# Optimization experiments

Hardware: AMD Instinct MI355X
Metric: run time of the kernel (lower is better)

Reference implementation:

```python
import jax, jax.numpy as jnp
import numpy as np

B, S, D_IN, D_OUT = 4, 2048, 1024, 1024

def setup_inputs() -> dict:
    key = jax.random.key(0)
    k_x, k_q, k_k, k_v = jax.random.split(key, 4)
    return {
        "x": jax.random.normal(k_x, (B, S, D_IN), dtype=jnp.float32),
        "W_query": jax.random.uniform(k_q, (D_IN, D_OUT), dtype=jnp.float32),
        "W_key": jax.random.uniform(k_k, (D_IN, D_OUT), dtype=jnp.float32),
        "W_value": jax.random.uniform(k_v, (D_IN, D_OUT), dtype=jnp.float32),
    }

def reference(x, W_query, W_key, W_value):
    seq_len = x.shape[1]
    d_out = W_key.shape[-1]
    # fused QKV projection: x @ concat([Wq, Wk, Wv], -1), then split
    qkv = x @ jnp.concatenate([W_query, W_key, W_value], axis=-1)  # [B,S,3*d_out]
    query, key, value = jnp.split(qkv, 3, axis=2)
    # raw scores [B,S,S]; causal mask applied BEFORE scaling (as in source)
    attn_weights = jnp.einsum("bqd,bkd->bqk", query, key)
    causal = jnp.triu(jnp.ones((seq_len, seq_len), dtype=bool), k=1)
    attn_weights = jnp.where(causal[None, :, :], -jnp.inf, attn_weights)
    scaled = attn_weights / jnp.asarray(d_out, x.dtype) ** 0.5
    attn_scores = jax.nn.softmax(scaled, axis=-1)  # dropout p=0 -> identity
    context_vectors = jnp.einsum("bqk,bkd->bqd", attn_scores, value)
    return (context_vectors, attn_scores)
```

## Files before the change

kernel.cpp:

```cpp
#include <hip/hip_runtime.h>
#include <cstdint>
#include <cstddef>


#define S_LEN 2048
#define D_DIM 1024
#define NBATCH 4
#define MEG (1024 * 1024)

typedef __attribute__((ext_vector_type(4))) float floatx4;
typedef __attribute__((ext_vector_type(8))) __bf16 bf16x8;
typedef __attribute__((ext_vector_type(8))) short short8v;

__device__ __forceinline__ unsigned short f2bf(float f) {
  union { float f; unsigned u; } v; v.f = f;
  unsigned r = v.u + 0x7FFF + ((v.u >> 16) & 1);
  return (unsigned short)(r >> 16);
}
__device__ __forceinline__ float bf2f(unsigned short h) {
  union { unsigned u; float f; } v; v.u = ((unsigned)h) << 16; return v.f;
}

__device__ __forceinline__ void async_copy16(const void* g, void* l) {
  __builtin_amdgcn_global_load_lds(
      (const __attribute__((address_space(1))) void*)g,
      (__attribute__((address_space(3))) void*)l, 16, 0, 0);
}

__device__ __forceinline__ void gemm_bt_core(
    const short* __restrict__ A, const short* __restrict__ B,
    int lda, int ldb, int kIters, int blockM, int blockN,
    short (*As)[32], short (*Bs)[32], floatx4 (&acc)[4][4])
{
  const int tid  = threadIdx.x;
  const int lane = tid & 63;
  const int wave = tid >> 6;
  const int wm = (wave >> 1) * 64;
  const int wn = (wave & 1) * 64;
  const int fm = lane & 15;
  const int fk = (lane >> 4) * 8;
  const int r0 = tid >> 2;
  const int c0 = (tid & 3) * 8;

  floatx4 zero = {0.f, 0.f, 0.f, 0.f};
  #pragma unroll
  for (int i = 0; i < 4; ++i)
    #pragma unroll
    for (int j = 0; j < 4; ++j)
      acc[i][j] = zero;

  const short* a0 = A + (size_t)(blockM + r0) * lda + c0;
  const short* a1 = a0 + (size_t)64 * lda;
  const short* b0 = B + (size_t)(blockN + r0) * ldb + c0;
  const short* b1 = b0 + (size_t)64 * ldb;
  short* as0 = &As[r0][c0];
  short* as1 = &As[r0 + 64][c0];
  short* bs0 = &Bs[r0][c0];
  short* bs1 = &Bs[r0 + 64][c0];

  for (int kt = 0; kt < kIters; ++kt) {
    const int kb = kt * 32;
    async_copy16(a0 + kb, as0);
    async_copy16(a1 + kb, as1);
    async_copy16(b0 + kb, bs0);
    async_copy16(b1 + kb, bs1);
    __syncthreads();
    bf16x8 af[4], bfr[4];
    #pragma unroll
    for (int i = 0; i < 4; ++i)
      af[i] = *(const bf16x8*)(&As[wm + i * 16 + fm][fk]);
    #pragma unroll
    for (int j = 0; j < 4; ++j)
      bfr[j] = *(const bf16x8*)(&Bs[wn + j * 16 + fm][fk]);
    #pragma unroll
    for (int i = 0; i < 4; ++i)
      #pragma unroll
      for (int j = 0; j < 4; ++j)
        acc[i][j] = __builtin_amdgcn_mfma_f32_16x16x32_bf16(af[i], bfr[j], acc[i][j], 0, 0, 0);
    __syncthreads();
  }
}

__device__ __forceinline__ void gemm_bt_split_core(
    const short* __restrict__ Ah, const short* __restrict__ Al,
    const short* __restrict__ Bh, const short* __restrict__ Bl,
    int lda, int ldb, int kIters, int blockM, int blockN,
    short (*AsH)[32], short (*AsL)[32], short (*BsH)[32], short (*BsL)[32],
    floatx4 (&acc)[4][4])
{
  const int tid  = threadIdx.x;
  const int lane = tid & 63;
  const int wave = tid >> 6;
  const int wm = (wave >> 1) * 64;
  const int wn = (wave & 1) * 64;
  const int fm = lane & 15;
  const int fk = (lane >> 4) * 8;
  const int r0 = tid >> 2;
  const int c0 = (tid & 3) * 8;

  floatx4 zero = {0.f, 0.f, 0.f, 0.f};
  #pragma unroll
  for (int i = 0; i < 4; ++i)
    #pragma unroll
    for (int j = 0; j < 4; ++j)
      acc[i][j] = zero;

  const size_t oa0 = (size_t)(blockM + r0) * lda + c0;
  const size_t oa1 = oa0 + (size_t)64 * lda;
  const size_t ob0 = (size_t)(blockN + r0) * ldb + c0;
  const size_t ob1 = ob0 + (size_t)64 * ldb;
  short* lah0 = &AsH[r0][c0]; short* lah1 = &AsH[r0 + 64][c0];
  short* lal0 = &AsL[r0][c0]; short* lal1 = &AsL[r0 + 64][c0];
  short* lbh0 = &BsH[r0][c0]; short* lbh1 = &BsH[r0 + 64][c0];
  short* lbl0 = &BsL[r0][c0]; short* lbl1 = &BsL[r0 + 64][c0];

  for (int kt = 0; kt < kIters; ++kt) {
    const int kb = kt * 32;
    async_copy16(Ah + oa0 + kb, lah0);
    async_copy16(Ah + oa1 + kb, lah1);
    async_copy16(Al + oa0 + kb, lal0);
    async_copy16(Al + oa1 + kb, lal1);
    async_copy16(Bh + ob0 + kb, lbh0);
    async_copy16(Bh + ob1 + kb, lbh1);
    async_copy16(Bl + ob0 + kb, lbl0);
    async_copy16(Bl + ob1 + kb, lbl1);
    __syncthreads();
    bf16x8 ah[4], al[4], bh[4], bl[4];
    #pragma unroll
    for (int i = 0; i < 4; ++i) {
      ah[i] = *(const bf16x8*)(&AsH[wm + i * 16 + fm][fk]);
      al[i] = *(const bf16x8*)(&AsL[wm + i * 16 + fm][fk]);
    }
    #pragma unroll
    for (int j = 0; j < 4; ++j) {
      bh[j] = *(const bf16x8*)(&BsH[wn + j * 16 + fm][fk]);
      bl[j] = *(const bf16x8*)(&BsL[wn + j * 16 + fm][fk]);
    }
    #pragma unroll
    for (int i = 0; i < 4; ++i)
      #pragma unroll
      for (int j = 0; j < 4; ++j) {
        acc[i][j] = __builtin_amdgcn_mfma_f32_16x16x32_bf16(ah[i], bh[j], acc[i][j], 0, 0, 0);
        acc[i][j] = __builtin_amdgcn_mfma_f32_16x16x32_bf16(ah[i], bl[j], acc[i][j], 0, 0, 0);
        acc[i][j] = __builtin_amdgcn_mfma_f32_16x16x32_bf16(al[i], bh[j], acc[i][j], 0, 0, 0);
      }
    __syncthreads();
  }
}


__global__ __launch_bounds__(256) void k_cvt(
    const float4* __restrict__ x,
    const float* __restrict__ wq, const float* __restrict__ wk,
    const float* __restrict__ wv,
    short* __restrict__ xh, short* __restrict__ xl,
    short* __restrict__ wqh, short* __restrict__ wql,
    short* __restrict__ wkh, short* __restrict__ wkl,
    short* __restrict__ wvt)
{
  const int bid = blockIdx.x;
  const int tid = threadIdx.x;
  if (bid < 5120) {
    const float4* src;
    short *dh, *dl;
    size_t idx;
    if (bid < 4096) {
      idx = (size_t)bid * 256 + tid;
      src = x; dh = xh; dl = xl;
    } else if (bid < 4608) {
      idx = (size_t)(bid - 4096) * 256 + tid;
      src = (const float4*)wq; dh = wqh; dl = wql;
    } else {
      idx = (size_t)(bid - 4608) * 256 + tid;
      src = (const float4*)wk; dh = wkh; dl = wkl;
    }
    const float4 u4 = src[idx * 2];
    const float4 w4 = src[idx * 2 + 1];
    float f[8] = {u4.x, u4.y, u4.z, u4.w, w4.x, w4.y, w4.z, w4.w};
    short8v oh, ol;
    #pragma unroll
    for (int e = 0; e < 8; ++e) {
      const unsigned short h = f2bf(f[e]);
      oh[e] = (short)h;
      ol[e] = (short)f2bf(f[e] - bf2f(h));
    }
    *(short8v*)(dh + idx * 8) = oh;
    *(short8v*)(dl + idx * 8) = ol;
  } else {
    const int rem = bid - 5120;
    const int bx = rem & 31, by = rem >> 5;
    const int tx = tid & 31, ty = tid >> 5;
    __shared__ float tile[32][33];
    const int colIn = bx * 32 + tx;
    #pragma unroll
    for (int i = 0; i < 4; ++i) {
      const int rowIn = by * 32 + ty + i * 8;
      tile[ty + i * 8][tx] = wv[(size_t)rowIn * D_DIM + colIn];
    }
    __syncthreads();
    const int colOut = by * 32 + tx;
    #pragma unroll
    for (int i = 0; i < 4; ++i) {
      const int rowOut = bx * 32 + ty + i * 8;
      wvt[(size_t)rowOut * D_DIM + colOut] = (short)f2bf(tile[tx][ty + i * 8]);
    }
  }
}


__global__ __launch_bounds__(256) void k_gemm_m(
    const short* __restrict__ wqh, const short* __restrict__ wql,
    const short* __restrict__ wkh, const short* __restrict__ wkl,
    short* __restrict__ mth, short* __restrict__ mtl)
{
  __shared__ alignas(16) short AsH[128][32];
  __shared__ alignas(16) short AsL[128][32];
  __shared__ alignas(16) short BsH[128][32];
  __shared__ alignas(16) short BsL[128][32];
  floatx4 acc[4][4];
  const int blockM = blockIdx.y * 128;
  const int blockN = blockIdx.x * 128;
  gemm_bt_split_core(wkh, wkl, wqh, wql,
                     D_DIM, D_DIM, D_DIM / 32, blockM, blockN,
                     AsH, AsL, BsH, BsL, acc);

  const int tid = threadIdx.x, lane = tid & 63, wave = tid >> 6;
  const int wm = (wave >> 1) * 64, wn = (wave & 1) * 64;
  const int rb = wm + ((lane >> 4) << 2);
  const int cb = wn + (lane & 15);
  #pragma unroll
  for (int i = 0; i < 4; ++i)
    #pragma unroll
    for (int j = 0; j < 4; ++j) {
      const int n = blockN + cb + j * 16;
      #pragma unroll
      for (int r = 0; r < 4; ++r) {
        const int m = blockM + rb + i * 16 + r;
        const float f = acc[i][j][r];
        const unsigned short h = f2bf(f);
        mth[(size_t)m * D_DIM + n] = (short)h;
        mtl[(size_t)m * D_DIM + n] = (short)f2bf(f - bf2f(h));
      }
    }
}


__global__ __launch_bounds__(256) void k_mu(const short* __restrict__ mth,
                                            const short* __restrict__ mtl,
                                            float* __restrict__ mu) {
  const int j = blockIdx.x, tid = threadIdx.x;
  const ushort4 h = *(const ushort4*)(mth + (size_t)j * D_DIM + tid * 4);
  const ushort4 l = *(const ushort4*)(mtl + (size_t)j * D_DIM + tid * 4);
  float s = bf2f(h.x) + bf2f(l.x) + bf2f(h.y) + bf2f(l.y)
          + bf2f(h.z) + bf2f(l.z) + bf2f(h.w) + bf2f(l.w);
  #pragma unroll
  for (int off = 32; off > 0; off >>= 1) s += __shfl_xor(s, off);
  __shared__ float ps[4];
  if ((tid & 63) == 0) ps[tid >> 6] = s;
  __syncthreads();
  if (tid == 0) mu[j] = (ps[0] + ps[1] + ps[2] + ps[3]) * (1.0f / 1024.0f);
}


__global__ __launch_bounds__(256) void k_rowstats(
    const short* __restrict__ xh, const short* __restrict__ xl,
    const float* __restrict__ mu, float* __restrict__ sq, float* __restrict__ u)
{
  const int r = blockIdx.x, tid = threadIdx.x;
  const ushort4 h = *(const ushort4*)(xh + (size_t)r * D_DIM + tid * 4);
  const ushort4 l = *(const ushort4*)(xl + (size_t)r * D_DIM + tid * 4);
  const float4 m4 = *(const float4*)(mu + tid * 4);
  const float x0 = bf2f(h.x) + bf2f(l.x);
  const float x1 = bf2f(h.y) + bf2f(l.y);
  const float x2 = bf2f(h.z) + bf2f(l.z);
  const float x3 = bf2f(h.w) + bf2f(l.w);
  float s = x0 + x1 + x2 + x3;
  float uu = m4.x * x0 + m4.y * x1 + m4.z * x2 + m4.w * x3;
  #pragma unroll
  for (int off = 32; off > 0; off >>= 1) {
    s  += __shfl_xor(s, off);
    uu += __shfl_xor(uu, off);
  }
  __shared__ float ps[4], pu[4];
  if ((tid & 63) == 0) { ps[tid >> 6] = s; pu[tid >> 6] = uu; }
  __syncthreads();
  if (tid == 0) {
    sq[r] = ps[0] + ps[1] + ps[2] + ps[3];
    u[r]  = pu[0] + pu[1] + pu[2] + pu[3];
  }
}


__global__ __launch_bounds__(256) void k_gemm_n(
    const short* __restrict__ xh, const short* __restrict__ xl,
    const short* __restrict__ mth, const short* __restrict__ mtl,
    const float* __restrict__ sq, const float* __restrict__ mu,
    short* __restrict__ nh, short* __restrict__ nl)
{
  __shared__ alignas(16) short AsH[128][32];
  __shared__ alignas(16) short AsL[128][32];
  __shared__ alignas(16) short BsH[128][32];
  __shared__ alignas(16) short BsL[128][32];
  floatx4 acc[4][4];
  const int blockM = blockIdx.y * 128;
  const int blockN = blockIdx.x * 128;
  gemm_bt_split_core(xh, xl, mth, mtl, D_DIM, D_DIM, D_DIM / 32,
                     blockM, blockN, AsH, AsL, BsH, BsL, acc);

  const int tid = threadIdx.x, lane = tid & 63, wave = tid >> 6;
  const int wm = (wave >> 1) * 64, wn = (wave & 1) * 64;
  const int rb = wm + ((lane >> 4) << 2);
  const int cb = wn + (lane & 15);
  #pragma unroll
  for (int i = 0; i < 4; ++i)
    #pragma unroll
    for (int j = 0; j < 4; ++j) {
      const int n = blockN + cb + j * 16;
      const float muv = mu[n];
      #pragma unroll
      for (int r = 0; r < 4; ++r) {
        const int m = blockM + rb + i * 16 + r;
        const float f = acc[i][j][r] - sq[m] * muv;
        const unsigned short h = f2bf(f);
        nh[(size_t)m * D_DIM + n] = (short)h;
        nl[(size_t)m * D_DIM + n] = (short)f2bf(f - bf2f(h));
      }
    }
}


__global__ __launch_bounds__(256) void k_gemm_sv(
    const short* __restrict__ nh, const short* __restrict__ nl,
    const short* __restrict__ xh, const short* __restrict__ xl,
    const float* __restrict__ sq, const float* __restrict__ u,
    const short* __restrict__ wvt, float* __restrict__ attn,
    short* __restrict__ vt)
{
  __shared__ alignas(16) short AsH[128][32];
  __shared__ alignas(16) short AsL[128][32];
  __shared__ alignas(16) short BsH[128][32];
  __shared__ alignas(16) short BsL[128][32];
  floatx4 acc[4][4];
  const int bid = blockIdx.x;
  const int tid = threadIdx.x, lane = tid & 63, wave = tid >> 6;
  const int wm = (wave >> 1) * 64, wn = (wave & 1) * 64;
  const int rb = wm + ((lane >> 4) << 2);
  const int cb = wn + (lane & 15);

  if (bid < 544) {
    const int b = bid / 136;
    int t = bid - b * 136, bi = 0;
    while (t >= bi + 1) { t -= bi + 1; ++bi; }
    const int bj = t;
    const size_t boff = (size_t)b * S_LEN * D_DIM;
    gemm_bt_split_core(nh + boff, nl + boff, xh + boff, xl + boff,
                       D_DIM, D_DIM, D_DIM / 32, bi * 128, bj * 128,
                       AsH, AsL, BsH, BsL, acc);

    float* out = attn + (size_t)b * S_LEN * S_LEN;
    const int rowBase = (b << 11) + bi * 128;
    const int colBase = (b << 11) + bj * 128;
    #pragma unroll
    for (int j = 0; j < 4; ++j) {
      const int n = bj * 128 + cb + j * 16;
      const float uv = u[colBase + cb + j * 16];
      #pragma unroll
      for (int i = 0; i < 4; ++i)
        #pragma unroll
        for (int r = 0; r < 4; ++r) {
          const int m = bi * 128 + rb + i * 16 + r;
          const float sv = sq[rowBase + rb + i * 16 + r];
          out[(size_t)m * S_LEN + n] = acc[i][j][r] + sv * uv;
        }
    }
  } else {
    const int vb = bid - 544;
    const int blockM = (vb >> 3) * 128;
    const int blockN = (vb & 7) * 128;
    gemm_bt_core(xh, wvt, D_DIM, D_DIM, D_DIM / 32, blockM, blockN,
                 AsH, BsH, acc);
    #pragma unroll
    for (int i = 0; i < 4; ++i)
      #pragma unroll
      for (int j = 0; j < 4; ++j) {
        const int n = blockN + cb + j * 16;
        const int m0 = blockM + rb + i * 16;
        const int b = m0 >> 11;
        const int s0 = m0 & (S_LEN - 1);
        ushort4 pk;
        pk.x = f2bf(acc[i][j][0]); pk.y = f2bf(acc[i][j][1]);
        pk.z = f2bf(acc[i][j][2]); pk.w = f2bf(acc[i][j][3]);
        *(ushort4*)(vt + ((size_t)b * D_DIM + n) * S_LEN + s0) = pk;
      }
  }
}


__global__ __launch_bounds__(256) void k_softmax(float* __restrict__ attn,
                                                 short* __restrict__ pb) {
  const int b = blockIdx.x >> 11;
  const int q = blockIdx.x & (S_LEN - 1);
  float* row  = attn + ((size_t)b * S_LEN + q) * S_LEN;
  short* prow = pb   + ((size_t)b * S_LEN + q) * S_LEN;
  const int tid = threadIdx.x;
  __shared__ float sMax[4], sSum[4];
  float v[8];
  float mx = -3.0e38f;
  #pragma unroll
  for (int e = 0; e < 8; ++e) {
    const int k = e * 256 + tid;
    v[e] = (k <= q) ? row[k] : -3.0e38f;
    mx = fmaxf(mx, v[e]);
  }
  #pragma unroll
  for (int off = 32; off > 0; off >>= 1) mx = fmaxf(mx, __shfl_xor(mx, off));
  if ((tid & 63) == 0) sMax[tid >> 6] = mx;
  __syncthreads();
  mx = fmaxf(fmaxf(sMax[0], sMax[1]), fmaxf(sMax[2], sMax[3]));

  float s = 0.f;
  #pragma unroll
  for (int e = 0; e < 8; ++e) {
    const int k = e * 256 + tid;
    const float p = (k <= q) ? __expf((v[e] - mx) * 0.03125f) : 0.f;
    v[e] = p;
    s += p;
  }
  #pragma unroll
  for (int off = 32; off > 0; off >>= 1) s += __shfl_xor(s, off);
  if ((tid & 63) == 0) sSum[tid >> 6] = s;
  __syncthreads();
  s = sSum[0] + sSum[1] + sSum[2] + sSum[3];
  const float inv = 1.0f / s;

  #pragma unroll
  for (int e = 0; e < 8; ++e) {
    const int k = e * 256 + tid;
    const float o = v[e] * inv;
    row[k] = o;
    prow[k] = (short)f2bf(o);
  }
}


__global__ __launch_bounds__(256) void k_gemm_ctx(
    const short* __restrict__ pb, const short* __restrict__ vt,
    float* __restrict__ ctx)
{
  __shared__ alignas(16) short As[128][32];
  __shared__ alignas(16) short Bs[128][32];
  floatx4 acc[4][4];
  const int b = blockIdx.z;
  const int by = 15 - blockIdx.y;
  const int blockM = by * 128;
  const int blockN = blockIdx.x * 128;
  const int kIters = by * 4 + 4;
  const short* A = pb + (size_t)b * S_LEN * S_LEN;
  const short* B = vt + (size_t)b * D_DIM * S_LEN;
  gemm_bt_core(A, B, S_LEN, S_LEN, kIters, blockM, blockN, As, Bs, acc);

  float* out = ctx + (size_t)b * S_LEN * D_DIM;
  const int tid = threadIdx.x, lane = tid & 63, wave = tid >> 6;
  const int wm = (wave >> 1) * 64, wn = (wave & 1) * 64;
  const int rb = wm + ((lane >> 4) << 2);
  const int cb = wn + (lane & 15);
  #pragma unroll
  for (int i = 0; i < 4; ++i)
    #pragma unroll
    for (int j = 0; j < 4; ++j) {
      const int n = blockN + cb + j * 16;
      #pragma unroll
      for (int r = 0; r < 4; ++r) {
        const int m = blockM + rb + i * 16 + r;
        out[(size_t)m * D_DIM + n] = acc[i][j][r];
      }
    }
}


extern "C" void kernel_launch(void* const* d_in, const int* in_sizes, int n_in,
                              void* d_out, int out_size, void* d_ws, size_t ws_size,
                              hipStream_t stream) {
  const float* x  = (const float*)d_in[0];
  const float* wq = (const float*)d_in[1];
  const float* wk = (const float*)d_in[2];
  const float* wv = (const float*)d_in[3];

  float* out  = (float*)d_out;
  float* ctx  = out;
  float* attn = out + (size_t)NBATCH * S_LEN * D_DIM;

  short* ws  = (short*)d_ws;
  short* xh  = ws;
  short* xl  = xh + (size_t)8 * MEG;
  short* wqh = xl + (size_t)8 * MEG;
  short* wql = wqh + (size_t)1 * MEG;
  short* wkh = wql + (size_t)1 * MEG;
  short* wkl = wkh + (size_t)1 * MEG;
  short* wvt = wkl + (size_t)1 * MEG;
  short* mth = wvt + (size_t)1 * MEG;
  short* mtl = mth + (size_t)1 * MEG;
  short* nh  = mtl + (size_t)1 * MEG;
  short* nl  = nh + (size_t)8 * MEG;
  short* vt  = nl + (size_t)8 * MEG;
  short* pb  = nh;
  float* fb  = (float*)(vt + (size_t)8 * MEG);
  float* mu  = fb;
  float* sq  = fb + 1024;
  float* u   = sq + 8192;

  k_cvt<<<6144, 256, 0, stream>>>((const float4*)x, wq, wk, wv,
                                  xh, xl, wqh, wql, wkh, wkl, wvt);
  k_gemm_m<<<dim3(8, 8), 256, 0, stream>>>(wqh, wql, wkh, wkl, mth, mtl);
  k_mu<<<1024, 256, 0, stream>>>(mth, mtl, mu);
  k_rowstats<<<8192, 256, 0, stream>>>(xh, xl, mu, sq, u);
  k_gemm_n<<<dim3(8, 64), 256, 0, stream>>>(xh, xl, mth, mtl, sq, mu, nh, nl);
  k_gemm_sv<<<1056, 256, 0, stream>>>(nh, nl, xh, xl, sq, u, wvt, attn, vt);
  k_softmax<<<NBATCH * S_LEN, 256, 0, stream>>>(attn, pb);
  k_gemm_ctx<<<dim3(8, 16, 4), 256, 0, stream>>>(pb, vt, ctx);
}
```

Measured before the change: 430.9 us.

## Use 256x256 tiles with atomic work queue in score/value GEMM kernel

```diff
diff --git a/kernel.cpp b/kernel.cpp
--- a/kernel.cpp
+++ b/kernel.cpp
@@ -7,6 +7,7 @@
 #define D_DIM 1024
 #define NBATCH 4
 #define MEG (1024 * 1024)
+#define SV_ITEMS 272
 
 typedef __attribute__((ext_vector_type(4))) float floatx4;
 typedef __attribute__((ext_vector_type(8))) __bf16 bf16x8;
@@ -26,6 +27,7 @@
       (const __attribute__((address_space(1))) void*)g,
       (__attribute__((address_space(3))) void*)l, 16, 0, 0);
 }
+
 
 __device__ __forceinline__ void gemm_bt_core(
     const short* __restrict__ A, const short* __restrict__ B,
@@ -144,6 +146,136 @@
         acc[i][j] = __builtin_amdgcn_mfma_f32_16x16x32_bf16(ah[i], bl[j], acc[i][j], 0, 0, 0);
         acc[i][j] = __builtin_amdgcn_mfma_f32_16x16x32_bf16(al[i], bh[j], acc[i][j], 0, 0, 0);
       }
+    __syncthreads();
+  }
+}
+
+
+__device__ __forceinline__ void gemm_bt_core512(
+    const short* __restrict__ A, const short* __restrict__ B,
+    int lda, int ldb, int kIters, int blockM, int blockN,
+    short (*As)[32], short (*Bs)[32], floatx4 (&acc)[4][8])
+{
+  const int tid  = threadIdx.x;
+  const int lane = tid & 63;
+  const int wave = tid >> 6;
+  const int wm = (wave >> 1) * 64;
+  const int wn = (wave & 1) * 128;
+  const int fm = lane & 15;
+  const int fk = (lane >> 4) * 8;
+  const int r0 = tid >> 2;
+  const int c0 = (tid & 3) * 8;
+
+  floatx4 zero = {0.f, 0.f, 0.f, 0.f};
+  #pragma unroll
+  for (int i = 0; i < 4; ++i)
+    #pragma unroll
+    for (int j = 0; j < 8; ++j)
+      acc[i][j] = zero;
+
+  const short* a0 = A + (size_t)(blockM + r0) * lda + c0;
+  const short* a1 = a0 + (size_t)128 * lda;
+  const short* b0 = B + (size_t)(blockN + r0) * ldb + c0;
+  const short* b1 = b0 + (size_t)128 * ldb;
+  short* as0 = &As[r0][c0];
+  short* as1 = &As[r0 + 128][c0];
+  short* bs0 = &Bs[r0][c0];
+  short* bs1 = &Bs[r0 + 128][c0];
+
+  for (int kt = 0; kt < kIters; ++kt) {
+    const int kb = kt * 32;
+    async_copy16(a0 + kb, as0);
+    async_copy16(a1 + kb, as1);
+    async_copy16(b0 + kb, bs0);
+    async_copy16(b1 + kb, bs1);
+    __syncthreads();
+    bf16x8 af[4], bfr[8];
+    #pragma unroll
+    for (int i = 0; i < 4; ++i)
+      af[i] = *(const bf16x8*)(&As[wm + i * 16 + fm][fk]);
+    #pragma unroll
+    for (int j = 0; j < 8; ++j)
+      bfr[j] = *(const bf16x8*)(&Bs[wn + j * 16 + fm][fk]);
+    #pragma unroll
+    for (int i = 0; i < 4; ++i)
+      #pragma unroll
+      for (int j = 0; j < 8; ++j)
+        acc[i][j] = __builtin_amdgcn_mfma_f32_16x16x32_bf16(af[i], bfr[j], acc[i][j], 0, 0, 0);
+    __syncthreads();
+  }
+}
+
+__device__ __forceinline__ void gemm_bt_split_core512(
+    const short* __restrict__ Ah, const short* __restrict__ Al,
+    const short* __restrict__ Bh, const short* __restrict__ Bl,
+    int lda, int ldb, int kIters, int blockM, int blockN,
+    short (*AsH)[32], short (*AsL)[32], short (*BsH)[32], short (*BsL)[32],
+    floatx4 (&acc)[4][8])
+{
+  const int tid  = threadIdx.x;
+  const int lane = tid & 63;
+  const int wave = tid >> 6;
+  const int wm = (wave >> 1) * 64;
+  const int wn = (wave & 1) * 128;
+  const int fm = lane & 15;
+  const int fk = (lane >> 4) * 8;
+  const int r0 = tid >> 2;
+  const int c0 = (tid & 3) * 8;
+
+  floatx4 zero = {0.f, 0.f, 0.f, 0.f};
+  #pragma unroll
+  for (int i = 0; i < 4; ++i)
+    #pragma unroll
+    for (int j = 0; j < 8; ++j)
+      acc[i][j] = zero;
+
+  const size_t oa0 = (size_t)(blockM + r0) * lda + c0;
+  const size_t oa1 = oa0 + (size_t)128 * lda;
+  const size_t ob0 = (size_t)(blockN + r0) * ldb + c0;
+  const size_t ob1 = ob0 + (size_t)128 * ldb;
+  short* lah0 = &AsH[r0][c0]; short* lah1 = &AsH[r0 + 128][c0];
+  short* lal0 = &AsL[r0][c0]; short* lal1 = &AsL[r0 + 128][c0];
+  short* lbh0 = &BsH[r0][c0]; short* lbh1 = &BsH[r0 + 128][c0];
+  short* lbl0 = &BsL[r0][c0]; short* lbl1 = &BsL[r0 + 128][c0];
+
+  for (int kt = 0; kt < kIters; ++kt) {
+    const int kb = kt * 32;
+    async_copy16(Ah + oa0 + kb, lah0);
+    async_copy16(Ah + oa1 + kb, lah1);
+    async_copy16(Al + oa0 + kb, lal0);
+    async_copy16(Al + oa1 + kb, lal1);
+    async_copy16(Bh + ob0 + kb, lbh0);
+    async_copy16(Bh + ob1 + kb, lbh1);
+    async_copy16(Bl + ob0 + kb, lbl0);
+    async_copy16(Bl + ob1 + kb, lbl1);
+    __syncthreads();
+    bf16x8 ah[4], bh[8], bl[8];
+    #pragma unroll
+    for (int i = 0; i < 4; ++i)
+      ah[i] = *(const bf16x8*)(&AsH[wm + i * 16 + fm][fk]);
+    #pragma unroll
+    for (int j = 0; j < 8; ++j)
+      bh[j] = *(const bf16x8*)(&BsH[wn + j * 16 + fm][fk]);
+    #pragma unroll
+    for (int i = 0; i < 4; ++i)
+      #pragma unroll
+      for (int j = 0; j < 8; ++j)
+        acc[i][j] = __builtin_amdgcn_mfma_f32_16x16x32_bf16(ah[i], bh[j], acc[i][j], 0, 0, 0);
+    #pragma unroll
+    for (int j = 0; j < 8; ++j)
+      bl[j] = *(const bf16x8*)(&BsL[wn + j * 16 + fm][fk]);
+    #pragma unroll
+    for (int i = 0; i < 4; ++i)
+      #pragma unroll
+      for (int j = 0; j < 8; ++j)
+        acc[i][j] = __builtin_amdgcn_mfma_f32_16x16x32_bf16(ah[i], bl[j], acc[i][j], 0, 0, 0);
+    #pragma unroll
+    for (int i = 0; i < 4; ++i) {
+      const bf16x8 al = *(const bf16x8*)(&AsL[wm + i * 16 + fm][fk]);
+      #pragma unroll
+      for (int j = 0; j < 8; ++j)
+        acc[i][j] = __builtin_amdgcn_mfma_f32_16x16x32_bf16(al, bh[j], acc[i][j], 0, 0, 0);
+    }
     __syncthreads();
   }
 }
@@ -264,9 +396,11 @@
 
 __global__ __launch_bounds__(256) void k_rowstats(
     const short* __restrict__ xh, const short* __restrict__ xl,
-    const float* __restrict__ mu, float* __restrict__ sq, float* __restrict__ u)
+    const float* __restrict__ mu, float* __restrict__ sq, float* __restrict__ u,
+    int* __restrict__ ctr)
 {
   const int r = blockIdx.x, tid = threadIdx.x;
+  if (r == 0 && tid == 0) *ctr = 0;
   const ushort4 h = *(const ushort4*)(xh + (size_t)r * D_DIM + tid * 4);
   const ushort4 l = *(const ushort4*)(xl + (size_t)r * D_DIM + tid * 4);
   const float4 m4 = *(const float4*)(mu + tid * 4);
@@ -329,69 +463,77 @@
 }
 
 
-__global__ __launch_bounds__(256) void k_gemm_sv(
+__global__ __launch_bounds__(512, 2) void k_gemm_sv512(
     const short* __restrict__ nh, const short* __restrict__ nl,
     const short* __restrict__ xh, const short* __restrict__ xl,
     const float* __restrict__ sq, const float* __restrict__ u,
     const short* __restrict__ wvt, float* __restrict__ attn,
-    short* __restrict__ vt)
-{
-  __shared__ alignas(16) short AsH[128][32];
-  __shared__ alignas(16) short AsL[128][32];
-  __shared__ alignas(16) short BsH[128][32];
-  __shared__ alignas(16) short BsL[128][32];
-  floatx4 acc[4][4];
-  const int bid = blockIdx.x;
+    short* __restrict__ vt, int* __restrict__ ctr)
+{
+  __shared__ alignas(16) short AsH[256][32];
+  __shared__ alignas(16) short AsL[256][32];
+  __shared__ alignas(16) short BsH[256][32];
+  __shared__ alignas(16) short BsL[256][32];
+  __shared__ int s_item;
+  floatx4 acc[4][8];
+
   const int tid = threadIdx.x, lane = tid & 63, wave = tid >> 6;
-  const int wm = (wave >> 1) * 64, wn = (wave & 1) * 64;
+  const int wm = (wave >> 1) * 64, wn = (wave & 1) * 128;
   const int rb = wm + ((lane >> 4) << 2);
   const int cb = wn + (lane & 15);
 
-  if (bid < 544) {
-    const int b = bid / 136;
-    int t = bid - b * 136, bi = 0;
-    while (t >= bi + 1) { t -= bi + 1; ++bi; }
-    const int bj = t;
-    const size_t boff = (size_t)b * S_LEN * D_DIM;
-    gemm_bt_split_core(nh + boff, nl + boff, xh + boff, xl + boff,
-                       D_DIM, D_DIM, D_DIM / 32, bi * 128, bj * 128,
-                       AsH, AsL, BsH, BsL, acc);
-
-    float* out = attn + (size_t)b * S_LEN * S_LEN;
-    const int rowBase = (b << 11) + bi * 128;
-    const int colBase = (b << 11) + bj * 128;
-    #pragma unroll
-    for (int j = 0; j < 4; ++j) {
-      const int n = bj * 128 + cb + j * 16;
-      const float uv = u[colBase + cb + j * 16];
+  for (;;) {
+    if (tid == 0) s_item = atomicAdd(ctr, 1);
+    __syncthreads();
+    const int it = s_item;
+    if (it >= SV_ITEMS) break;
+
+    if (it < 144) {
+      const int b = it / 36;
+      int t = it - b * 36, bi = 0;
+      while (t >= bi + 1) { t -= bi + 1; ++bi; }
+      const int bj = t;
+      const size_t boff = (size_t)b * S_LEN * D_DIM;
+      gemm_bt_split_core512(nh + boff, nl + boff, xh + boff, xl + boff,
+                            D_DIM, D_DIM, D_DIM / 32, bi * 256, bj * 256,
+                            AsH, AsL, BsH, BsL, acc);
+
+      float* out = attn + (size_t)b * S_LEN * S_LEN;
+      const int rowBase = (b << 11) + bi * 256;
+      const int colBase = (b << 11) + bj * 256;
+      #pragma unroll
+      for (int j = 0; j < 8; ++j) {
+        const int n = bj * 256 + cb + j * 16;
+        const float uv = u[colBase + cb + j * 16];
+        #pragma unroll
+        for (int i = 0; i < 4; ++i)
+          #pragma unroll
+          for (int r = 0; r < 4; ++r) {
+            const int m = bi * 256 + rb + i * 16 + r;
+            const float sv = sq[rowBase + rb + i * 16 + r];
+            out[(size_t)m * S_LEN + n] = acc[i][j][r] + sv * uv;
+          }
+      }
+    } else {
+      const int vb = it - 144;
+      const int blockM = (vb >> 2) * 256;
+      const int blockN = (vb & 3) * 256;
+      gemm_bt_core512(xh, wvt, D_DIM, D_DIM, D_DIM / 32, blockM, blockN,
+                      AsH, BsH, acc);
       #pragma unroll
       for (int i = 0; i < 4; ++i)
         #pragma unroll
-        for (int r = 0; r < 4; ++r) {
-          const int m = bi * 128 + rb + i * 16 + r;
-          const float sv = sq[rowBase + rb + i * 16 + r];
-          out[(size_t)m * S_LEN + n] = acc[i][j][r] + sv * uv;
+        for (int j = 0; j < 8; ++j) {
+          const int n = blockN + cb + j * 16;
+          const int m0 = blockM + rb + i * 16;
+          const int b = m0 >> 11;
+          const int s0 = m0 & (S_LEN - 1);
+          ushort4 pk;
+          pk.x = f2bf(acc[i][j][0]); pk.y = f2bf(acc[i][j][1]);
+          pk.z = f2bf(acc[i][j][2]); pk.w = f2bf(acc[i][j][3]);
+          *(ushort4*)(vt + ((size_t)b * D_DIM + n) * S_LEN + s0) = pk;
         }
     }
-  } else {
-    const int vb = bid - 544;
-    const int blockM = (vb >> 3) * 128;
-    const int blockN = (vb & 7) * 128;
-    gemm_bt_core(xh, wvt, D_DIM, D_DIM, D_DIM / 32, blockM, blockN,
-                 AsH, BsH, acc);
-    #pragma unroll
-    for (int i = 0; i < 4; ++i)
-      #pragma unroll
-      for (int j = 0; j < 4; ++j) {
-        const int n = blockN + cb + j * 16;
-        const int m0 = blockM + rb + i * 16;
-        const int b = m0 >> 11;
-        const int s0 = m0 & (S_LEN - 1);
-        ushort4 pk;
-        pk.x = f2bf(acc[i][j][0]); pk.y = f2bf(acc[i][j][1]);
-        pk.z = f2bf(acc[i][j][2]); pk.w = f2bf(acc[i][j][3]);
-        *(ushort4*)(vt + ((size_t)b * D_DIM + n) * S_LEN + s0) = pk;
-      }
   }
 }
 
@@ -508,14 +650,15 @@
   float* mu  = fb;
   float* sq  = fb + 1024;
   float* u   = sq + 8192;
+  int*   ctr = (int*)(u + 8192);
 
   k_cvt<<<6144, 256, 0, stream>>>((const float4*)x, wq, wk, wv,
                                   xh, xl, wqh, wql, wkh, wkl, wvt);
   k_gemm_m<<<dim3(8, 8), 256, 0, stream>>>(wqh, wql, wkh, wkl, mth, mtl);
   k_mu<<<1024, 256, 0, stream>>>(mth, mtl, mu);
-  k_rowstats<<<8192, 256, 0, stream>>>(xh, xl, mu, sq, u);
+  k_rowstats<<<8192, 256, 0, stream>>>(xh, xl, mu, sq, u, ctr);
   k_gemm_n<<<dim3(8, 64), 256, 0, stream>>>(xh, xl, mth, mtl, sq, mu, nh, nl);
-  k_gemm_sv<<<1056, 256, 0, stream>>>(nh, nl, xh, xl, sq, u, wvt, attn, vt);
+  k_gemm_sv512<<<512, 512, 0, stream>>>(nh, nl, xh, xl, sq, u, wvt, attn, vt, ctr);
   k_softmax<<<NBATCH * S_LEN, 256, 0, stream>>>(attn, pb);
   k_gemm_ctx<<<dim3(8, 16, 4), 256, 0, stream>>>(pb, vt, ctx);
 }
```

Result: faster. 399.3 us (-7.3%).

## Fuse mu into gemm_m epilogue, co-schedule V with N gemm, rebalance S and ctx grids

Applied to the files above, without the earlier changes.

```diff
diff --git a/kernel.cpp b/kernel.cpp
--- a/kernel.cpp
+++ b/kernel.cpp
@@ -26,6 +26,7 @@
       (const __attribute__((address_space(1))) void*)g,
       (__attribute__((address_space(3))) void*)l, 16, 0, 0);
 }
+
 
 __device__ __forceinline__ void gemm_bt_core(
     const short* __restrict__ A, const short* __restrict__ B,
@@ -156,7 +157,7 @@
     short* __restrict__ xh, short* __restrict__ xl,
     short* __restrict__ wqh, short* __restrict__ wql,
     short* __restrict__ wkh, short* __restrict__ wkl,
-    short* __restrict__ wvt)
+    short* __restrict__ wvt, float* __restrict__ muSum)
 {
   const int bid = blockIdx.x;
   const int tid = threadIdx.x;
@@ -187,6 +188,10 @@
     *(short8v*)(dh + idx * 8) = oh;
     *(short8v*)(dl + idx * 8) = ol;
   } else {
+    if (bid == 5120) {
+      float4 z = {0.f, 0.f, 0.f, 0.f};
+      ((float4*)muSum)[tid] = z;
+    }
     const int rem = bid - 5120;
     const int bx = rem & 31, by = rem >> 5;
     const int tx = tid & 31, ty = tid >> 5;
@@ -211,7 +216,8 @@
 __global__ __launch_bounds__(256) void k_gemm_m(
     const short* __restrict__ wqh, const short* __restrict__ wql,
     const short* __restrict__ wkh, const short* __restrict__ wkl,
-    short* __restrict__ mth, short* __restrict__ mtl)
+    short* __restrict__ mth, short* __restrict__ mtl,
+    float* __restrict__ muSum)
 {
   __shared__ alignas(16) short AsH[128][32];
   __shared__ alignas(16) short AsL[128][32];
@@ -242,34 +248,27 @@
         mtl[(size_t)m * D_DIM + n] = (short)f2bf(f - bf2f(h));
       }
     }
-}
-
-
-__global__ __launch_bounds__(256) void k_mu(const short* __restrict__ mth,
-                                            const short* __restrict__ mtl,
-                                            float* __restrict__ mu) {
-  const int j = blockIdx.x, tid = threadIdx.x;
-  const ushort4 h = *(const ushort4*)(mth + (size_t)j * D_DIM + tid * 4);
-  const ushort4 l = *(const ushort4*)(mtl + (size_t)j * D_DIM + tid * 4);
-  float s = bf2f(h.x) + bf2f(l.x) + bf2f(h.y) + bf2f(l.y)
-          + bf2f(h.z) + bf2f(l.z) + bf2f(h.w) + bf2f(l.w);
-  #pragma unroll
-  for (int off = 32; off > 0; off >>= 1) s += __shfl_xor(s, off);
-  __shared__ float ps[4];
-  if ((tid & 63) == 0) ps[tid >> 6] = s;
-  __syncthreads();
-  if (tid == 0) mu[j] = (ps[0] + ps[1] + ps[2] + ps[3]) * (1.0f / 1024.0f);
+  #pragma unroll
+  for (int i = 0; i < 4; ++i)
+    #pragma unroll
+    for (int r = 0; r < 4; ++r) {
+      float v = acc[i][0][r] + acc[i][1][r] + acc[i][2][r] + acc[i][3][r];
+      v += __shfl_xor(v, 1); v += __shfl_xor(v, 2);
+      v += __shfl_xor(v, 4); v += __shfl_xor(v, 8);
+      if ((lane & 15) == 0)
+        atomicAdd(&muSum[blockM + rb + i * 16 + r], v);
+    }
 }
 
 
 __global__ __launch_bounds__(256) void k_rowstats(
     const short* __restrict__ xh, const short* __restrict__ xl,
-    const float* __restrict__ mu, float* __restrict__ sq, float* __restrict__ u)
+    const float* __restrict__ muSum, float* __restrict__ sq, float* __restrict__ u)
 {
   const int r = blockIdx.x, tid = threadIdx.x;
   const ushort4 h = *(const ushort4*)(xh + (size_t)r * D_DIM + tid * 4);
   const ushort4 l = *(const ushort4*)(xl + (size_t)r * D_DIM + tid * 4);
-  const float4 m4 = *(const float4*)(mu + tid * 4);
+  const float4 m4 = *(const float4*)(muSum + tid * 4);
   const float x0 = bf2f(h.x) + bf2f(l.x);
   const float x1 = bf2f(h.y) + bf2f(l.y);
   const float x2 = bf2f(h.z) + bf2f(l.z);
@@ -286,97 +285,54 @@
   __syncthreads();
   if (tid == 0) {
     sq[r] = ps[0] + ps[1] + ps[2] + ps[3];
-    u[r]  = pu[0] + pu[1] + pu[2] + pu[3];
-  }
-}
-
-
-__global__ __launch_bounds__(256) void k_gemm_n(
+    u[r]  = (pu[0] + pu[1] + pu[2] + pu[3]) * (1.0f / 1024.0f);
+  }
+}
+
+
+__global__ __launch_bounds__(256) void k_gemm_nv(
     const short* __restrict__ xh, const short* __restrict__ xl,
     const short* __restrict__ mth, const short* __restrict__ mtl,
-    const float* __restrict__ sq, const float* __restrict__ mu,
-    short* __restrict__ nh, short* __restrict__ nl)
+    const float* __restrict__ sq, const float* __restrict__ muSum,
+    const short* __restrict__ wvt,
+    short* __restrict__ nh, short* __restrict__ nl, short* __restrict__ vt)
 {
   __shared__ alignas(16) short AsH[128][32];
   __shared__ alignas(16) short AsL[128][32];
   __shared__ alignas(16) short BsH[128][32];
   __shared__ alignas(16) short BsL[128][32];
   floatx4 acc[4][4];
-  const int blockM = blockIdx.y * 128;
-  const int blockN = blockIdx.x * 128;
-  gemm_bt_split_core(xh, xl, mth, mtl, D_DIM, D_DIM, D_DIM / 32,
-                     blockM, blockN, AsH, AsL, BsH, BsL, acc);
+
+  const int g = blockIdx.x;
+  const int id = (g & 7) * 128 + (g >> 3);
+  const int idx = id >> 1;
+  const int blockM = (idx >> 3) * 128;
+  const int blockN = (idx & 7) * 128;
 
   const int tid = threadIdx.x, lane = tid & 63, wave = tid >> 6;
   const int wm = (wave >> 1) * 64, wn = (wave & 1) * 64;
   const int rb = wm + ((lane >> 4) << 2);
   const int cb = wn + (lane & 15);
-  #pragma unroll
-  for (int i = 0; i < 4; ++i)
-    #pragma unroll
-    for (int j = 0; j < 4; ++j) {
-      const int n = blockN + cb + j * 16;
-      const float muv = mu[n];
-      #pragma unroll
-      for (int r = 0; r < 4; ++r) {
-        const int m = blockM + rb + i * 16 + r;
-        const float f = acc[i][j][r] - sq[m] * muv;
-        const unsigned short h = f2bf(f);
-        nh[(size_t)m * D_DIM + n] = (short)h;
-        nl[(size_t)m * D_DIM + n] = (short)f2bf(f - bf2f(h));
-      }
-    }
-}
-
-
-__global__ __launch_bounds__(256) void k_gemm_sv(
-    const short* __restrict__ nh, const short* __restrict__ nl,
-    const short* __restrict__ xh, const short* __restrict__ xl,
-    const float* __restrict__ sq, const float* __restrict__ u,
-    const short* __restrict__ wvt, float* __restrict__ attn,
-    short* __restrict__ vt)
-{
-  __shared__ alignas(16) short AsH[128][32];
-  __shared__ alignas(16) short AsL[128][32];
-  __shared__ alignas(16) short BsH[128][32];
-  __shared__ alignas(16) short BsL[128][32];
-  floatx4 acc[4][4];
-  const int bid = blockIdx.x;
-  const int tid = threadIdx.x, lane = tid & 63, wave = tid >> 6;
-  const int wm = (wave >> 1) * 64, wn = (wave & 1) * 64;
-  const int rb = wm + ((lane >> 4) << 2);
-  const int cb = wn + (lane & 15);
-
-  if (bid < 544) {
-    const int b = bid / 136;
-    int t = bid - b * 136, bi = 0;
-    while (t >= bi + 1) { t -= bi + 1; ++bi; }
-    const int bj = t;
-    const size_t boff = (size_t)b * S_LEN * D_DIM;
-    gemm_bt_split_core(nh + boff, nl + boff, xh + boff, xl + boff,
-                       D_DIM, D_DIM, D_DIM / 32, bi * 128, bj * 128,
-                       AsH, AsL, BsH, BsL, acc);
-
-    float* out = attn + (size_t)b * S_LEN * S_LEN;
-    const int rowBase = (b << 11) + bi * 128;
-    const int colBase = (b << 11) + bj * 128;
-    #pragma unroll
-    for (int j = 0; j < 4; ++j) {
-      const int n = bj * 128 + cb + j * 16;
-      const float uv = u[colBase + cb + j * 16];
-      #pragma unroll
-      for (int i = 0; i < 4; ++i)
+
+  if ((id & 1) == 0) {
+    gemm_bt_split_core(xh, xl, mth, mtl, D_DIM, D_DIM, D_DIM / 32,
+                       blockM, blockN, AsH, AsL, BsH, BsL, acc);
+    #pragma unroll
+    for (int i = 0; i < 4; ++i)
+      #pragma unroll
+      for (int j = 0; j < 4; ++j) {
+        const int n = blockN + cb + j * 16;
+        const float muv = muSum[n] * (1.0f / 1024.0f);
         #pragma unroll
         for (int r = 0; r < 4; ++r) {
-          const int m = bi * 128 + rb + i * 16 + r;
-          const float sv = sq[rowBase + rb + i * 16 + r];
-          out[(size_t)m * S_LEN + n] = acc[i][j][r] + sv * uv;
+          const int m = blockM + rb + i * 16 + r;
+          const float f = acc[i][j][r] - sq[m] * muv;
+          const unsigned short h = f2bf(f);
+          nh[(size_t)m * D_DIM + n] = (short)h;
+          nl[(size_t)m * D_DIM + n] = (short)f2bf(f - bf2f(h));
         }
-    }
+      }
   } else {
-    const int vb = bid - 544;
-    const int blockM = (vb >> 3) * 128;
-    const int blockN = (vb & 7) * 128;
     gemm_bt_core(xh, wvt, D_DIM, D_DIM, D_DIM / 32, blockM, blockN,
                  AsH, BsH, acc);
     #pragma unroll
@@ -396,6 +352,61 @@
 }
 
 
+__global__ __launch_bounds__(256) void k_gemm_s(
+    const short* __restrict__ nh, const short* __restrict__ nl,
+    const short* __restrict__ xh, const short* __restrict__ xl,
+    const float* __restrict__ sq, const float* __restrict__ u,
+    float* __restrict__ attn)
+{
+  __shared__ alignas(16) short AsH[128][32];
+  __shared__ alignas(16) short AsL[128][32];
+  __shared__ alignas(16) short BsH[128][32];
+  __shared__ alignas(16) short BsL[128][32];
+  floatx4 acc[4][4];
+
+  const int g = blockIdx.x;
+  const int item = (g & 7) * 68 + (g >> 3);
+  const int b = item / 136;
+  int t = item - b * 136;
+  int band = 0;
+  while (t >= 58 - 16 * band) { t -= 58 - 16 * band; ++band; }
+  int bi = band * 4;
+  for (;;) {
+    const int w = bi - band * 4 + 1;
+    const int ww = w < 4 ? w : 4;
+    if (t < ww) break;
+    t -= ww; ++bi;
+  }
+  const int bj = band * 4 + t;
+
+  const size_t boff = (size_t)b * S_LEN * D_DIM;
+  gemm_bt_split_core(nh + boff, nl + boff, xh + boff, xl + boff,
+                     D_DIM, D_DIM, D_DIM / 32, bi * 128, bj * 128,
+                     AsH, AsL, BsH, BsL, acc);
+
+  float* out = attn + (size_t)b * S_LEN * S_LEN;
+  const int tid = threadIdx.x, lane = tid & 63, wave = tid >> 6;
+  const int wm = (wave >> 1) * 64, wn = (wave & 1) * 64;
+  const int rb = wm + ((lane >> 4) << 2);
+  const int cb = wn + (lane & 15);
+  const int rowBase = (b << 11) + bi * 128;
+  const int colBase = (b << 11) + bj * 128;
+  #pragma unroll
+  for (int j = 0; j < 4; ++j) {
+    const int n = bj * 128 + cb + j * 16;
+    const float uv = u[colBase + cb + j * 16];
+    #pragma unroll
+    for (int i = 0; i < 4; ++i)
+      #pragma unroll
+      for (int r = 0; r < 4; ++r) {
+        const int m = bi * 128 + rb + i * 16 + r;
+        const float sv = sq[rowBase + rb + i * 16 + r];
+        out[(size_t)m * S_LEN + n] = acc[i][j][r] + sv * uv;
+      }
+  }
+}
+
+
 __global__ __launch_bounds__(256) void k_softmax(float* __restrict__ attn,
                                                  short* __restrict__ pb) {
   const int b = blockIdx.x >> 11;
@@ -448,26 +459,63 @@
     float* __restrict__ ctx)
 {
   __shared__ alignas(16) short As[128][32];
-  __shared__ alignas(16) short Bs[128][32];
-  floatx4 acc[4][4];
+  __shared__ alignas(16) short Bs[64][32];
+  floatx4 acc[4][2];
   const int b = blockIdx.z;
   const int by = 15 - blockIdx.y;
   const int blockM = by * 128;
-  const int blockN = blockIdx.x * 128;
+  const int blockN = blockIdx.x * 64;
   const int kIters = by * 4 + 4;
   const short* A = pb + (size_t)b * S_LEN * S_LEN;
   const short* B = vt + (size_t)b * D_DIM * S_LEN;
-  gemm_bt_core(A, B, S_LEN, S_LEN, kIters, blockM, blockN, As, Bs, acc);
+
+  const int tid = threadIdx.x, lane = tid & 63, wave = tid >> 6;
+  const int wm = (wave >> 1) * 64, wn = (wave & 1) * 32;
+  const int fm = lane & 15, fk = (lane >> 4) * 8;
+  const int r0 = tid >> 2, c0 = (tid & 3) * 8;
+
+  floatx4 zero = {0.f, 0.f, 0.f, 0.f};
+  #pragma unroll
+  for (int i = 0; i < 4; ++i)
+    #pragma unroll
+    for (int j = 0; j < 2; ++j)
+      acc[i][j] = zero;
+
+  const short* a0 = A + (size_t)(blockM + r0) * S_LEN + c0;
+  const short* a1 = a0 + (size_t)64 * S_LEN;
+  const short* b0 = B + (size_t)(blockN + r0) * S_LEN + c0;
+  short* as0 = &As[r0][c0];
+  short* as1 = &As[r0 + 64][c0];
+  short* bs0 = &Bs[r0][c0];
+
+  for (int kt = 0; kt < kIters; ++kt) {
+    const int kb = kt * 32;
+    async_copy16(a0 + kb, as0);
+    async_copy16(a1 + kb, as1);
+    async_copy16(b0 + kb, bs0);
+    __syncthreads();
+    bf16x8 af[4], bfr[2];
+    #pragma unroll
+    for (int i = 0; i < 4; ++i)
+      af[i] = *(const bf16x8*)(&As[wm + i * 16 + fm][fk]);
+    #pragma unroll
+    for (int j = 0; j < 2; ++j)
+      bfr[j] = *(const bf16x8*)(&Bs[wn + j * 16 + fm][fk]);
+    #pragma unroll
+    for (int i = 0; i < 4; ++i)
+      #pragma unroll
+      for (int j = 0; j < 2; ++j)
+        acc[i][j] = __builtin_amdgcn_mfma_f32_16x16x32_bf16(af[i], bfr[j], acc[i][j], 0, 0, 0);
+    __syncthreads();
+  }
 
   float* out = ctx + (size_t)b * S_LEN * D_DIM;
-  const int tid = threadIdx.x, lane = tid & 63, wave = tid >> 6;
-  const int wm = (wave >> 1) * 64, wn = (wave & 1) * 64;
   const int rb = wm + ((lane >> 4) << 2);
   const int cb = wn + (lane & 15);
   #pragma unroll
   for (int i = 0; i < 4; ++i)
     #pragma unroll
-    for (int j = 0; j < 4; ++j) {
+    for (int j = 0; j < 2; ++j) {
       const int n = blockN + cb + j * 16;
       #pragma unroll
       for (int r = 0; r < 4; ++r) {
@@ -505,17 +553,16 @@
   short* vt  = nl + (size_t)8 * MEG;
   short* pb  = nh;
   float* fb  = (float*)(vt + (size_t)8 * MEG);
-  float* mu  = fb;
+  float* muS = fb;
   float* sq  = fb + 1024;
   float* u   = sq + 8192;
 
   k_cvt<<<6144, 256, 0, stream>>>((const float4*)x, wq, wk, wv,
-                                  xh, xl, wqh, wql, wkh, wkl, wvt);
-  k_gemm_m<<<dim3(8, 8), 256, 0, stream>>>(wqh, wql, wkh, wkl, mth, mtl);
-  k_mu<<<1024, 256, 0, stream>>>(mth, mtl, mu);
-  k_rowstats<<<8192, 256, 0, stream>>>(xh, xl, mu, sq, u);
-  k_gemm_n<<<dim3(8, 64), 256, 0, stream>>>(xh, xl, mth, mtl, sq, mu, nh, nl);
-  k_gemm_sv<<<1056, 256, 0, stream>>>(nh, nl, xh, xl, sq, u, wvt, attn, vt);
+                                  xh, xl, wqh, wql, wkh, wkl, wvt, muS);
+  k_gemm_m<<<dim3(8, 8), 256, 0, stream>>>(wqh, wql, wkh, wkl, mth, mtl, muS);
+  k_rowstats<<<8192, 256, 0, stream>>>(xh, xl, muS, sq, u);
+  k_gemm_nv<<<1024, 256, 0, stream>>>(xh, xl, mth, mtl, sq, muS, wvt, nh, nl, vt);
+  k_gemm_s<<<544, 256, 0, stream>>>(nh, nl, xh, xl, sq, u, attn);
   k_softmax<<<NBATCH * S_LEN, 256, 0, stream>>>(attn, pb);
-  k_gemm_ctx<<<dim3(8, 16, 4), 256, 0, stream>>>(pb, vt, ctx);
-}
+  k_gemm_ctx<<<dim3(16, 16, 4), 256, 0, stream>>>(pb, vt, ctx);
+}
```

New measurement: 428.9 us. Within noise of the previous version (-0.5%).
